# Performance work log

Measured on AMD Instinct MI355X. Metric: run time of the kernel, lower is better.

## Reference

```python
import jax, jax.numpy as jnp
from jax import lax
import numpy as np

IN, G, H, L = 128, 5, 512, 256   # input_size, n_genres, hidden_dim, latent_dim
E = 2 * H                         # encoder_hidden_dim (bidirectional)
B, T = 128, 256
SLOPE = 0.01                      # torch LeakyReLU default


def _gru(xt, h, Wih, Whh, bih, bhh):
    # torch.nn.GRUCell: gates ordered r, z, n
    gi = xt @ Wih.T + bih         # [B, 3H]
    gh = h @ Whh.T + bhh          # [B, 3H]
    ir, iz, inn = jnp.split(gi, 3, axis=-1)
    hr, hz, hn = jnp.split(gh, 3, axis=-1)
    r = jax.nn.sigmoid(ir + hr)
    z = jax.nn.sigmoid(iz + hz)
    n = jnp.tanh(inn + r * hn)
    return (1.0 - z) * n + z * h


def _leaky(v):
    return jnp.where(v >= 0, v, SLOPE * v)


def setup_inputs() -> dict:
    key = jax.random.key(0)
    ks = jax.random.split(key, 32)
    it = iter(range(32))

    def p(shape, fan_in):
        s = 1.0 / np.sqrt(fan_in)
        return jax.random.uniform(ks[next(it)], shape, jnp.float32, -s, s)

    inp = {
        "x": jax.random.normal(ks[next(it)], (B, T, IN + G), jnp.float32),
        "latent_genre_vec": jax.random.uniform(ks[next(it)], (B, G), jnp.float32),
        "eps": jax.random.normal(ks[next(it)], (B, L - G), jnp.float32),
    }
    # forward encoder GRUCell (input IN+G -> H)
    inp["Wih_e"] = p((3 * H, IN + G), H); inp["Whh_e"] = p((3 * H, H), H)
    inp["bih_e"] = p((3 * H,), H);        inp["bhh_e"] = p((3 * H,), H)
    # backward encoder GRUCell
    inp["Wih_be"] = p((3 * H, IN + G), H); inp["Whh_be"] = p((3 * H, H), H)
    inp["bih_be"] = p((3 * H,), H);        inp["bhh_be"] = p((3 * H,), H)
    # decoder GRUCell (input IN -> H)
    inp["Wih_d"] = p((3 * H, IN), H); inp["Whh_d"] = p((3 * H, H), H)
    inp["bih_d"] = p((3 * H,), H);    inp["bhh_d"] = p((3 * H,), H)
    # fc_mu: [Linear(E,E)+LeakyReLU, Linear(E, L-G)]
    inp["W_mu0"] = p((E, E), E); inp["b_mu0"] = p((E,), E)
    inp["W_mu1"] = p((L - G, E), E); inp["b_mu1"] = p((L - G,), E)
    # fc_logvar
    inp["W_lv0"] = p((E, E), E); inp["b_lv0"] = p((E,), E)
    inp["W_lv1"] = p((L - G, E), E); inp["b_lv1"] = p((L - G,), E)
    # fc_latent: [Linear(L,L)+LeakyReLU, Linear(L, H)]
    inp["W_lat0"] = p((L, L), L); inp["b_lat0"] = p((L,), L)
    inp["W_lat1"] = p((H, L), L); inp["b_lat1"] = p((H,), L)
    # fc_decoder final Linear(H, IN) (fc_decoder[0] is dead code in the original loop)
    inp["W_dec1"] = p((IN, H), H); inp["b_dec1"] = p((IN,), H)
    return inp


def reference(x, latent_genre_vec, eps,
              Wih_e, Whh_e, bih_e, bhh_e,
              Wih_be, Whh_be, bih_be, bhh_be,
              Wih_d, Whh_d, bih_d, bhh_d,
              W_mu0, b_mu0, W_mu1, b_mu1,
              W_lv0, b_lv0, W_lv1, b_lv1,
              W_lat0, b_lat0, W_lat1, b_lat1,
              W_dec1, b_dec1):
    b = x.shape[0]
    xs = jnp.swapaxes(x, 0, 1)  # [T, B, IN+G]
    h0 = jnp.zeros((b, H), x.dtype)

    def enc_step(h, xt):
        return _gru(xt, h, Wih_e, Whh_e, bih_e, bhh_e), None

    def benc_step(h, xt):
        return _gru(xt, h, Wih_be, Whh_be, bih_be, bhh_be), None

    h_fwd, _ = lax.scan(enc_step, h0, xs)
    h_bwd, _ = lax.scan(benc_step, h0, xs, reverse=True)
    hidden = jnp.concatenate([h_fwd, h_bwd], axis=1)  # [B, 2H]

    mu = _leaky(hidden @ W_mu0.T + b_mu0) @ W_mu1.T + b_mu1        # [B, L-G]
    logvar = _leaky(hidden @ W_lv0.T + b_lv0) @ W_lv1.T + b_lv1    # [B, L-G]

    z = mu + jnp.exp(0.5 * logvar) * eps
    z = jnp.concatenate([z, latent_genre_vec], axis=1)             # [B, L]

    dec_h = _leaky(z @ W_lat0.T + b_lat0) @ W_lat1.T + b_lat1      # [B, H]

    note0 = x[:, 0, :IN]  # [B, IN]

    def dec_step(carry, _):
        h, note = carry
        h = _gru(note, h, Wih_d, Whh_d, bih_d, bhh_d)
        # faithful to original: final fc_decoder layer applied to hidden
        note = h @ W_dec1.T + b_dec1
        return (h, note), note

    _, notes = lax.scan(dec_step, (dec_h, note0), None, length=x.shape[1] - 1)
    output = jnp.concatenate([note0[:, None, :], jnp.swapaxes(notes, 0, 1)], axis=1)  # [B, T, IN]
    return output, mu, logvar
```

## Files before the change

kernel.cpp:

```cpp
#include <hip/hip_runtime.h>

#define B_ 128
#define T_ 256
#define IN_ 128
#define G_ 5
#define H_ 512
#define G3_ 1536
#define E_ 1024
#define L_ 256
#define LG_ 251
#define INPG_ 133

#define MU_OFF (B_*T_*IN_)
#define LV_OFF (MU_OFF + B_*LG_)

typedef __attribute__((ext_vector_type(8))) short bf16x8;
typedef __attribute__((ext_vector_type(4))) float f32x4;
typedef unsigned long long u64;

__device__ __forceinline__ float bf2f(unsigned short s) {
    return __uint_as_float(((unsigned)s) << 16);
}
__device__ __forceinline__ unsigned short f2bf(float f) {
    unsigned x = __float_as_uint(f);
    unsigned r = (x + 0x7fffu + ((x >> 16) & 1u)) >> 16;
    return (unsigned short)r;
}
__device__ __forceinline__ float sigf(float v) {
    return 1.f / (1.f + __expf(-v));
}
__device__ __forceinline__ int ld_flag(const int* p) {
    return __hip_atomic_load(p, __ATOMIC_RELAXED, __HIP_MEMORY_SCOPE_AGENT);
}
__device__ __forceinline__ void st_flag(int* p, int v) {
    __hip_atomic_store(p, v, __ATOMIC_RELAXED, __HIP_MEMORY_SCOPE_AGENT);
}
__device__ __forceinline__ u64 ld_h64(const void* p) {
    return __hip_atomic_load((const u64*)p, __ATOMIC_RELAXED, __HIP_MEMORY_SCOPE_AGENT);
}
__device__ __forceinline__ void st_h32(void* p, unsigned v) {
    __hip_atomic_store((unsigned*)p, v, __ATOMIC_RELAXED, __HIP_MEMORY_SCOPE_AGENT);
}


__global__ void xpad_k(const float* __restrict__ x, ushort* __restrict__ xb) {
    int id = blockIdx.x * 256 + threadIdx.x;
    if (id >= T_ * B_ * 160) return;
    int t = id / (B_ * 160);
    int rem = id - t * (B_ * 160);
    int b = rem / 160, c = rem - b * 160;
    float v = (c < INPG_) ? x[((size_t)b * T_ + t) * INPG_ + c] : 0.f;
    xb[id] = f2bf(v);
}

__global__ void pack_we(const float* __restrict__ Wih_f, const float* __restrict__ Whh_f,
                        const float* __restrict__ Wih_b, const float* __restrict__ Whh_b,
                        ushort* __restrict__ WE) {
    int id = blockIdx.x * 256 + threadIdx.x;
    int lane = id & 63;
    int rest = id >> 6;
    int ks = rest % 63;
    int cb = (rest / 63) & 31;
    int dir = rest / (63 * 32);
    if (dir >= 2) return;
    const float* Wih = dir ? Wih_b : Wih_f;
    const float* Whh = dir ? Whh_b : Whh_f;
    int n = lane & 15, kb = lane >> 4;
    int p, ksp;
    if (ks < 21)      { p = 0; ksp = ks; }
    else if (ks < 42) { p = 1; ksp = ks - 21; }
    else if (ks < 47) { p = 2; ksp = ks - 42; }
    else              { p = 3; ksp = ks - 47; }
    int j = cb * 16 + n;
    int row = (p == 0) ? j : (p == 1) ? 512 + j : 1024 + j;
    #pragma unroll
    for (int e = 0; e < 8; ++e) {
        int k = ksp * 32 + kb * 8 + e;
        float v;
        if (p == 3)      v = Whh[(size_t)row * 512 + k];
        else if (p == 2) v = (k < INPG_) ? Wih[(size_t)row * INPG_ + k] : 0.f;
        else v = (k < INPG_) ? Wih[(size_t)row * INPG_ + k]
               : (k < 160)   ? 0.f
               : Whh[(size_t)row * 512 + (k - 160)];
        WE[(size_t)id * 8 + e] = f2bf(v);
    }
}

__global__ void wfused_k(const float* __restrict__ Wih_d, const float* __restrict__ Wdec1,
                         float* __restrict__ Wf) {
    int id = blockIdx.x * 256 + threadIdx.x;
    if (id >= G3_ * H_) return;
    int r = id >> 9, c = id & 511;
    float s = 0.f;
    for (int m = 0; m < 128; ++m)
        s += Wih_d[(size_t)r * 128 + m] * Wdec1[(size_t)m * 512 + c];
    Wf[id] = s;
}

__global__ void bfi_k(const float* __restrict__ Wih_d, const float* __restrict__ b_dec1,
                      const float* __restrict__ bih_d, float* __restrict__ bfi) {
    int r = blockIdx.x * 256 + threadIdx.x;
    if (r >= G3_) return;
    float s = bih_d[r];
    for (int m = 0; m < 128; ++m)
        s += Wih_d[(size_t)r * 128 + m] * b_dec1[m];
    bfi[r] = s;
}

__global__ void pack_wd(const float* __restrict__ Wf, const float* __restrict__ Whh,
                        ushort* __restrict__ WD, int fused) {
    int id = blockIdx.x * 256 + threadIdx.x;
    int lane = id & 63;
    int rest = id >> 6;
    int ks = rest & 63;
    int cb = rest >> 6;
    if (cb >= 32) return;
    int p = ks >> 4, ksp = ks & 15;
    int n = lane & 15, kb = lane >> 4;
    int j = cb * 16 + n;
    int row = (p == 0) ? j : (p == 1) ? 512 + j : 1024 + j;
    #pragma unroll
    for (int e = 0; e < 8; ++e) {
        int k = ksp * 32 + kb * 8 + e;
        float v;
        if (p <= 1) v = fused ? (Wf[(size_t)row * 512 + k] + Whh[(size_t)row * 512 + k])
                              : Whh[(size_t)row * 512 + k];
        else if (p == 2) v = fused ? Wf[(size_t)row * 512 + k] : 0.f;
        else v = Whh[(size_t)row * 512 + k];
        WD[(size_t)id * 8 + e] = f2bf(v);
    }
}

__global__ void pack_wdec(const float* __restrict__ Wdec1, ushort* __restrict__ pk) {
    int id = blockIdx.x * 256 + threadIdx.x;
    if (id >= 8192) return;
    int lane = id & 63, ch = id >> 6;
    int nt = ch >> 4, ks = ch & 15;
    int n = nt * 16 + (lane & 15);
    int k0 = ks * 32 + (lane >> 4) * 8;
    #pragma unroll
    for (int e = 0; e < 8; ++e)
        pk[(size_t)id * 8 + e] = f2bf(Wdec1[(size_t)n * 512 + k0 + e]);
}

__global__ void zero_init(ushort* __restrict__ hb, int* __restrict__ ef,
                          int* __restrict__ df) {
    int id = blockIdx.x * 256 + threadIdx.x;
    if (id < 4 * 65536) hb[id] = 0;
    if (id < 4096) ef[id] = 0;
    if (id < 2048) df[id] = 0;
}

__global__ void note0_k2(const float* __restrict__ x, float* __restrict__ out,
                         float* __restrict__ note0f) {
    int id = blockIdx.x * 256 + threadIdx.x;
    if (id >= B_ * IN_) return;
    int b = id >> 7, n = id & 127;
    float v = x[((size_t)b * T_) * INPG_ + n];
    out[((size_t)b * T_) * IN_ + n] = v;
    note0f[(size_t)b * 128 + n] = v;
}

__global__ void cvt_h0(const float* __restrict__ src, ushort* __restrict__ dst) {
    int id = blockIdx.x * 256 + threadIdx.x;
    if (id < B_ * H_) dst[id] = f2bf(src[id]);
}

__global__ void tile_w(const float* __restrict__ W, ushort4* __restrict__ out,
                       int N, int K, int KC) {
    int id = blockIdx.x * 256 + threadIdx.x;
    if (id >= KC * N) return;
    int kc = id / N, n = id - kc * N;
    int k = kc * 4;
    ushort4 u;
    u.x = f2bf(k + 0 < K ? W[(size_t)n * K + k + 0] : 0.f);
    u.y = f2bf(k + 1 < K ? W[(size_t)n * K + k + 1] : 0.f);
    u.z = f2bf(k + 2 < K ? W[(size_t)n * K + k + 2] : 0.f);
    u.w = f2bf(k + 3 < K ? W[(size_t)n * K + k + 3] : 0.f);
    out[(size_t)kc * N + n] = u;
}

__global__ __launch_bounds__(256) void enc_persist(
    const ushort* __restrict__ xb16, const ushort* __restrict__ WE,
    ushort* __restrict__ hb,
    float* __restrict__ hidden,
    const float* __restrict__ bih_f, const float* __restrict__ bhh_f,
    const float* __restrict__ bih_b, const float* __restrict__ bhh_b,
    int* __restrict__ flags)
{
    __shared__ ushort As[32 * 680];
    __shared__ ushort Ws[63 * 512];
    __shared__ float gs[4][512];
    int bid = blockIdx.x;
    int dir = bid >> 7, bt = (bid >> 5) & 3, cb = bid & 31;
    int b0 = bt * 32;
    int tid = threadIdx.x;
    const float* bih = dir ? bih_b : bih_f;
    const float* bhh = dir ? bhh_b : bhh_f;

    {
        const ushort* src = WE + (size_t)((dir * 32 + cb) * 63) * 512;
        for (int c = tid; c < 4032; c += 256)
            *(uint4*)&Ws[c * 8] = *(const uint4*)&src[c * 8];
    }
    int bA = tid >> 3;
    int j0 = cb * 16 + 2 * (tid & 7), j1 = j0 + 1;
    float b_r0 = bih[j0] + bhh[j0],        b_r1 = bih[j1] + bhh[j1];
    float b_z0 = bih[512 + j0] + bhh[512 + j0], b_z1 = bih[512 + j1] + bhh[512 + j1];
    float b_in0 = bih[1024 + j0],          b_in1 = bih[1024 + j1];
    float b_hn0 = bhh[1024 + j0],          b_hn1 = bhh[1024 + j1];
    float hc0 = 0.f, hc1 = 0.f;

    int lane = tid & 63, wv = tid >> 6;
    int m = lane & 15, kb = lane >> 4;
    int nk  = (wv == 2) ? 5 : (wv == 3) ? 16 : 21;
    int ksb = (wv == 0) ? 0 : (wv == 1) ? 21 : (wv == 2) ? 42 : 47;
    int kcol0 = (wv == 3) ? 160 : 0;
    int ai0 = m * 680 + kcol0 + kb * 8;
    int ai1 = (16 + m) * 680 + kcol0 + kb * 8;
    const int* fpoll = &flags[((bid & ~31) + (lane & 31)) * 16];

    auto stage_x = [&](int t2) {
        int tt2 = dir ? (255 - t2) : t2;
        const ushort* xr2 = xb16 + (size_t)tt2 * (B_ * 160);
        #pragma unroll
        for (int i = 0; i < 3; ++i) {
            int c = tid + i * 256;
            if (c < 640) {
                int row = c / 20, off = c - row * 20;
                *(uint4*)((char*)As + row * 1360 + off * 16) =
                    *(const uint4*)(xr2 + (size_t)(b0 + row) * 160 + off * 8);
            }
        }
    };
    stage_x(0);

    for (int t = 0; t < T_; ++t) {
        int pp = t & 1;
        const ushort* hin = hb + (size_t)(pp * 2 + dir) * 65536;
        ushort* hout = hb + (size_t)((pp ^ 1) * 2 + dir) * 65536;
        if (t > 0) {
            if (wv == 0)
                while (!__all(ld_flag(fpoll) >= t)) __builtin_amdgcn_s_sleep(1);
            __syncthreads();
        }
        {
            u64 vb[16];
            #pragma unroll
            for (int i = 0; i < 16; ++i) {
                int c = tid + i * 256;
                int row = c >> 7, off = c & 127;
                vb[i] = ld_h64(hin + (size_t)(b0 + row) * 512 + off * 4);
            }
            #pragma unroll
            for (int i = 0; i < 16; ++i) {
                int c = tid + i * 256;
                int row = c >> 7, off = c & 127;
                *(u64*)((char*)As + row * 1360 + 320 + off * 8) = vb[i];
            }
        }
        __syncthreads();
        f32x4 acc0 = {0.f,0.f,0.f,0.f}, acc1 = {0.f,0.f,0.f,0.f};
        const ushort* Bp = &Ws[ksb * 512 + lane * 8];
        for (int ks = 0; ks < nk; ++ks) {
            bf16x8 bfr = *(const bf16x8*)(Bp + (size_t)ks * 512);
            bf16x8 a0 = *(const bf16x8*)&As[ai0 + ks * 32];
            bf16x8 a1 = *(const bf16x8*)&As[ai1 + ks * 32];
            acc0 = __builtin_amdgcn_mfma_f32_16x16x32_bf16(a0, bfr, acc0, 0, 0, 0);
            acc1 = __builtin_amdgcn_mfma_f32_16x16x32_bf16(a1, bfr, acc1, 0, 0, 0);
        }
        #pragma unroll
        for (int i = 0; i < 4; ++i) {
            gs[wv][(kb * 4 + i) * 16 + m] = acc0[i];
            gs[wv][(16 + kb * 4 + i) * 16 + m] = acc1[i];
        }
        __syncthreads();
        {
            int o0 = 2 * tid, o1 = o0 + 1;
            float r0 = sigf(gs[0][o0] + b_r0);
            float z0 = sigf(gs[1][o0] + b_z0);
            float n0 = tanhf(gs[2][o0] + b_in0 + r0 * (gs[3][o0] + b_hn0));
            hc0 = (1.f - z0) * n0 + z0 * hc0;
            float r1 = sigf(gs[0][o1] + b_r1);
            float z1 = sigf(gs[1][o1] + b_z1);
            float n1 = tanhf(gs[2][o1] + b_in1 + r1 * (gs[3][o1] + b_hn1));
            hc1 = (1.f - z1) * n1 + z1 * hc1;
            unsigned pkd = (unsigned)f2bf(hc0) | ((unsigned)f2bf(hc1) << 16);
            st_h32((char*)hout + ((size_t)(b0 + bA) * 512 + j0) * 2, pkd);
            if (t == 255) {
                float2 hv = {hc0, hc1};
                *(float2*)&hidden[(size_t)(b0 + bA) * 1024 + dir * 512 + j0] = hv;
            }
        }
        __syncthreads();
        if (t < 255) {
            if (tid == 0) st_flag(&flags[bid * 16], t + 1);
            stage_x(t + 1);
        }
    }
}

__global__ __launch_bounds__(256) void dec_persist(
    const ushort* __restrict__ hdec0, const ushort* __restrict__ WD2,
    const ushort* __restrict__ WD1, ushort* __restrict__ hist,
    const float* __restrict__ h0f, const float* __restrict__ bfi,
    const float* __restrict__ bhh, const float* __restrict__ gi0,
    int* __restrict__ flags)
{
    __shared__ ushort As[32 * 520];
    __shared__ ushort Ws[64 * 512];
    __shared__ float gs[4][512];
    int bid = blockIdx.x;
    int bt = bid >> 5, cb = bid & 31;
    int b0 = bt * 32, tid = threadIdx.x;
    {
        const ushort* src = WD2 + (size_t)(cb * 64) * 512;
        for (int c = tid; c < 4096; c += 256)
            *(uint4*)&Ws[c * 8] = *(const uint4*)&src[c * 8];
    }
    int bA = tid >> 3;
    int j0 = cb * 16 + 2 * (tid & 7), j1 = j0 + 1;
    float f_r0 = bfi[j0] + bhh[j0],             f_r1 = bfi[j1] + bhh[j1];
    float f_z0 = bfi[512 + j0] + bhh[512 + j0], f_z1 = bfi[512 + j1] + bhh[512 + j1];
    float f_in0 = bfi[1024 + j0],               f_in1 = bfi[1024 + j1];
    float f_hn0 = bhh[1024 + j0],               f_hn1 = bhh[1024 + j1];
    float bh_r0 = bhh[j0], bh_r1 = bhh[j1];
    float bh_z0 = bhh[512 + j0], bh_z1 = bhh[512 + j1];
    float hc0 = h0f[(size_t)(b0 + bA) * 512 + j0];
    float hc1 = h0f[(size_t)(b0 + bA) * 512 + j1];
    float g0r = gi0[(size_t)(b0 + bA) * G3_ + j0];
    float g1r = gi0[(size_t)(b0 + bA) * G3_ + j1];
    float g0z = gi0[(size_t)(b0 + bA) * G3_ + 512 + j0];
    float g1z = gi0[(size_t)(b0 + bA) * G3_ + 512 + j1];
    float g0n = gi0[(size_t)(b0 + bA) * G3_ + 1024 + j0];
    float g1n = gi0[(size_t)(b0 + bA) * G3_ + 1024 + j1];

    int lane = tid & 63, wv = tid >> 6;
    int m = lane & 15, kb = lane >> 4;
    int ai0 = m * 520 + kb * 8, ai1 = (16 + m) * 520 + kb * 8;
    const ushort* WD1s = WD1 + (size_t)(cb * 64 + wv * 16) * 512 + lane * 8;
    const int* fpoll = &flags[((bid & ~31) + (lane & 31)) * 16];

    for (int t = 1; t < T_; ++t) {
        if (t >= 2) {
            if (wv == 0)
                while (!__all(ld_flag(fpoll) >= t - 1)) __builtin_amdgcn_s_sleep(1);
            __syncthreads();
        }
        const ushort* hsrc = (t == 1) ? hdec0 : hist + (size_t)(t - 2) * 65536;
        {
            u64 vb[16];
            #pragma unroll
            for (int i = 0; i < 16; ++i) {
                int c = tid + i * 256;
                int row = c >> 7, off = c & 127;
                vb[i] = ld_h64(hsrc + (size_t)(b0 + row) * 512 + off * 4);
            }
            #pragma unroll
            for (int i = 0; i < 16; ++i) {
                int c = tid + i * 256;
                int row = c >> 7, off = c & 127;
                *(u64*)((char*)As + row * 1040 + off * 8) = vb[i];
            }
        }
        __syncthreads();
        f32x4 acc0 = {0.f,0.f,0.f,0.f}, acc1 = {0.f,0.f,0.f,0.f};
        if (t == 1) {
            if (wv != 2) {
                for (int ks = 0; ks < 16; ++ks) {
                    bf16x8 bfr = *(const bf16x8*)(WD1s + (size_t)ks * 512);
                    bf16x8 a0 = *(const bf16x8*)&As[ai0 + ks * 32];
                    bf16x8 a1 = *(const bf16x8*)&As[ai1 + ks * 32];
                    acc0 = __builtin_amdgcn_mfma_f32_16x16x32_bf16(a0, bfr, acc0, 0, 0, 0);
                    acc1 = __builtin_amdgcn_mfma_f32_16x16x32_bf16(a1, bfr, acc1, 0, 0, 0);
                }
            }
        } else {
            const ushort* Bp = &Ws[(wv * 16) * 512 + lane * 8];
            for (int ks = 0; ks < 16; ++ks) {
                bf16x8 bfr = *(const bf16x8*)(Bp + (size_t)ks * 512);
                bf16x8 a0 = *(const bf16x8*)&As[ai0 + ks * 32];
                bf16x8 a1 = *(const bf16x8*)&As[ai1 + ks * 32];
                acc0 = __builtin_amdgcn_mfma_f32_16x16x32_bf16(a0, bfr, acc0, 0, 0, 0);
                acc1 = __builtin_amdgcn_mfma_f32_16x16x32_bf16(a1, bfr, acc1, 0, 0, 0);
            }
        }
        #pragma unroll
        for (int i = 0; i < 4; ++i) {
            gs[wv][(kb * 4 + i) * 16 + m] = acc0[i];
            gs[wv][(16 + kb * 4 + i) * 16 + m] = acc1[i];
        }
        __syncthreads();
        {
            int o0 = 2 * tid, o1 = o0 + 1;
            float r0, z0, n0, r1, z1, n1;
            if (t == 1) {
                r0 = sigf(gs[0][o0] + g0r + bh_r0);
                z0 = sigf(gs[1][o0] + g0z + bh_z0);
                n0 = tanhf(gs[2][o0] + g0n + r0 * (gs[3][o0] + f_hn0));
                r1 = sigf(gs[0][o1] + g1r + bh_r1);
                z1 = sigf(gs[1][o1] + g1z + bh_z1);
                n1 = tanhf(gs[2][o1] + g1n + r1 * (gs[3][o1] + f_hn1));
            } else {
                r0 = sigf(gs[0][o0] + f_r0);
                z0 = sigf(gs[1][o0] + f_z0);
                n0 = tanhf(gs[2][o0] + f_in0 + r0 * (gs[3][o0] + f_hn0));
                r1 = sigf(gs[0][o1] + f_r1);
                z1 = sigf(gs[1][o1] + f_z1);
                n1 = tanhf(gs[2][o1] + f_in1 + r1 * (gs[3][o1] + f_hn1));
            }
            hc0 = (1.f - z0) * n0 + z0 * hc0;
            hc1 = (1.f - z1) * n1 + z1 * hc1;
            unsigned pkd = (unsigned)f2bf(hc0) | ((unsigned)f2bf(hc1) << 16);
            st_h32((char*)(hist + (size_t)(t - 1) * 65536) +
                   ((size_t)(b0 + bA) * 512 + j0) * 2, pkd);
        }
        __syncthreads();
        if (t < 255 && tid == 0) st_flag(&flags[bid * 16], t);
    }
}

__global__ __launch_bounds__(256) void notes_mfma(
    const ushort* __restrict__ hist, const ushort* __restrict__ pk,
    const float* __restrict__ bd, float* __restrict__ out)
{
    __shared__ ushort hs[32 * 520];
    int m0 = blockIdx.x * 32;
    int tid = threadIdx.x;
    #pragma unroll
    for (int i = 0; i < 8; ++i) {
        int c = tid + i * 256;
        int row = c >> 6, off = c & 63;
        *(uint4*)((char*)hs + row * 1040 + off * 16) =
            *(const uint4*)(hist + (size_t)(m0 + row) * 512 + off * 8);
    }
    __syncthreads();
    int lane = tid & 63, wv = tid >> 6;
    int m = lane & 15, kb = lane >> 4;
    int nt0 = wv * 2;
    f32x4 acc00 = {0.f,0.f,0.f,0.f}, acc01 = {0.f,0.f,0.f,0.f};
    f32x4 acc10 = {0.f,0.f,0.f,0.f}, acc11 = {0.f,0.f,0.f,0.f};
    for (int ks = 0; ks < 16; ++ks) {
        bf16x8 a0 = *(const bf16x8*)&hs[m * 520 + ks * 32 + kb * 8];
        bf16x8 a1 = *(const bf16x8*)&hs[(16 + m) * 520 + ks * 32 + kb * 8];
        bf16x8 bf0 = *(const bf16x8*)&pk[(size_t)((nt0 * 16 + ks) * 64 + lane) * 8];
        bf16x8 bf1 = *(const bf16x8*)&pk[(size_t)(((nt0 + 1) * 16 + ks) * 64 + lane) * 8];
        acc00 = __builtin_amdgcn_mfma_f32_16x16x32_bf16(a0, bf0, acc00, 0, 0, 0);
        acc01 = __builtin_amdgcn_mfma_f32_16x16x32_bf16(a0, bf1, acc01, 0, 0, 0);
        acc10 = __builtin_amdgcn_mfma_f32_16x16x32_bf16(a1, bf0, acc10, 0, 0, 0);
        acc11 = __builtin_amdgcn_mfma_f32_16x16x32_bf16(a1, bf1, acc11, 0, 0, 0);
    }
    int n0 = nt0 * 16 + (lane & 15), n1 = (nt0 + 1) * 16 + (lane & 15);
    #pragma unroll
    for (int i = 0; i < 4; ++i) {
        int r0 = m0 + kb * 4 + i;
        int r1 = r0 + 16;
        int t0 = r0 >> 7, b0r = r0 & 127;
        int t1 = r1 >> 7, b1r = r1 & 127;
        out[((size_t)b0r * T_ + (t0 + 1)) * IN_ + n0] = acc00[i] + bd[n0];
        out[((size_t)b0r * T_ + (t0 + 1)) * IN_ + n1] = acc01[i] + bd[n1];
        out[((size_t)b1r * T_ + (t1 + 1)) * IN_ + n0] = acc10[i] + bd[n0];
        out[((size_t)b1r * T_ + (t1 + 1)) * IN_ + n1] = acc11[i] + bd[n1];
    }
}

__global__ __launch_bounds__(256) void gemm_t4(
    const float* __restrict__ A, const ushort4* __restrict__ Wt,
    const float* __restrict__ bias, float* __restrict__ C,
    int M, int N, int K, int act)
{
    int nb = blockIdx.x, mb = blockIdx.y;
    int tid = threadIdx.x;
    int n = nb * 64 + (tid & 63);
    int mq = tid >> 6;
    int m0 = mb * 32;
    __shared__ float Asm[32][36];
    float acc[8];
    #pragma unroll
    for (int i = 0; i < 8; ++i) acc[i] = 0.f;
    for (int k0 = 0; k0 < K; k0 += 32) {
        int r = tid >> 3, c = (tid & 7) << 2;
        float4 v = *(const float4*)&A[(size_t)(m0 + r) * K + k0 + c];
        Asm[r][c] = v.x; Asm[r][c+1] = v.y; Asm[r][c+2] = v.z; Asm[r][c+3] = v.w;
        __syncthreads();
        #pragma unroll
        for (int kc = 0; kc < 8; ++kc) {
            float w0 = 0.f, w1 = 0.f, w2 = 0.f, w3 = 0.f;
            if (n < N) {
                ushort4 u = Wt[(size_t)((k0 >> 2) + kc) * N + n];
                w0 = bf2f(u.x); w1 = bf2f(u.y); w2 = bf2f(u.z); w3 = bf2f(u.w);
            }
            #pragma unroll
            for (int i = 0; i < 8; ++i) {
                int mm = mq * 8 + i;
                acc[i] += Asm[mm][kc*4+0]*w0 + Asm[mm][kc*4+1]*w1
                        + Asm[mm][kc*4+2]*w2 + Asm[mm][kc*4+3]*w3;
            }
        }
        __syncthreads();
    }
    if (n < N) {
        #pragma unroll
        for (int i = 0; i < 8; ++i) {
            int mm = m0 + mq * 8 + i;
            float v = acc[i] + bias[n];
            if (act == 1) v = (v >= 0.f) ? v : 0.01f * v;
            C[(size_t)mm * N + n] = v;
        }
    }
}

__global__ void z_k(const float* __restrict__ out, const float* __restrict__ eps,
                    const float* __restrict__ genre, float* __restrict__ zc) {
    int id = blockIdx.x * 256 + threadIdx.x;
    if (id >= B_ * L_) return;
    int b = id >> 8, c = id & 255;
    float v;
    if (c < LG_) {
        float mu = out[MU_OFF + (size_t)b * LG_ + c];
        float lv = out[LV_OFF + (size_t)b * LG_ + c];
        v = mu + expf(0.5f * lv) * eps[(size_t)b * LG_ + c];
    } else {
        v = genre[(size_t)b * G_ + (c - LG_)];
    }
    zc[id] = v;
}

extern "C" void kernel_launch(void* const* d_in, const int* in_sizes, int n_in,
                              void* d_out, int out_size, void* d_ws, size_t ws_size,
                              hipStream_t stream) {
    (void)in_sizes; (void)n_in; (void)out_size; (void)ws_size;
    const float* x      = (const float*)d_in[0];
    const float* genre  = (const float*)d_in[1];
    const float* eps    = (const float*)d_in[2];
    const float* Wih_e  = (const float*)d_in[3];
    const float* Whh_e  = (const float*)d_in[4];
    const float* bih_e  = (const float*)d_in[5];
    const float* bhh_e  = (const float*)d_in[6];
    const float* Wih_be = (const float*)d_in[7];
    const float* Whh_be = (const float*)d_in[8];
    const float* bih_be = (const float*)d_in[9];
    const float* bhh_be = (const float*)d_in[10];
    const float* Wih_d  = (const float*)d_in[11];
    const float* Whh_d  = (const float*)d_in[12];
    const float* bih_d  = (const float*)d_in[13];
    const float* bhh_d  = (const float*)d_in[14];
    const float* W_mu0  = (const float*)d_in[15];
    const float* b_mu0  = (const float*)d_in[16];
    const float* W_mu1  = (const float*)d_in[17];
    const float* b_mu1  = (const float*)d_in[18];
    const float* W_lv0  = (const float*)d_in[19];
    const float* b_lv0  = (const float*)d_in[20];
    const float* W_lv1  = (const float*)d_in[21];
    const float* b_lv1  = (const float*)d_in[22];
    const float* W_lat0 = (const float*)d_in[23];
    const float* b_lat0 = (const float*)d_in[24];
    const float* W_lat1 = (const float*)d_in[25];
    const float* b_lat1 = (const float*)d_in[26];
    const float* W_dec1 = (const float*)d_in[27];
    const float* b_dec1 = (const float*)d_in[28];
    float* out = (float*)d_out;

    char* ws = (char*)d_ws;
    size_t off = 0;
    auto alloc = [&](size_t bytes) -> char* {
        char* p = ws + off;
        off = (off + bytes + 255) & ~(size_t)255;
        return p;
    };
    ushort* xb16  = (ushort*)alloc((size_t)T_ * B_ * 160 * 2);
    ushort* WE    = (ushort*)alloc((size_t)2 * 32 * 63 * 512 * 2);
    ushort* WD2   = (ushort*)alloc((size_t)32 * 64 * 512 * 2);
    ushort* WD1   = (ushort*)alloc((size_t)32 * 64 * 512 * 2);
    float*  Wf    = (float*)alloc((size_t)G3_ * H_ * 4);
    float*  bfi   = (float*)alloc(G3_ * 4);
    ushort* hb_e  = (ushort*)alloc((size_t)4 * 65536 * 2);
    ushort* hist  = (ushort*)alloc((size_t)255 * 65536 * 2);
    ushort* hdec0 = (ushort*)alloc((size_t)65536 * 2);
    ushort* pkdec = (ushort*)alloc((size_t)8192 * 8 * 2);
    int*    eflag = (int*)alloc((size_t)4096 * 4);
    int*    dflag = (int*)alloc((size_t)2048 * 4);
    float*  note0f= (float*)alloc((size_t)B_ * 128 * 4);
    float*  gi0   = (float*)alloc((size_t)B_ * G3_ * 4);
    float*  hidden= (float*)alloc((size_t)B_ * E_ * 4);
    float*  t0buf = (float*)alloc((size_t)B_ * E_ * 4);
    float*  t1buf = (float*)alloc((size_t)B_ * E_ * 4);
    float*  zcbuf = (float*)alloc((size_t)B_ * L_ * 4);
    float*  t2buf = (float*)alloc((size_t)B_ * L_ * 4);
    float*  t3buf = (float*)alloc((size_t)B_ * H_ * 4);

    ushort4* T_Wmu0  = (ushort4*)alloc((size_t)256 * E_ * 8);
    ushort4* T_Wmu1  = (ushort4*)alloc((size_t)256 * LG_ * 8);
    ushort4* T_Wlv0  = (ushort4*)alloc((size_t)256 * E_ * 8);
    ushort4* T_Wlv1  = (ushort4*)alloc((size_t)256 * LG_ * 8);
    ushort4* T_Wlat0 = (ushort4*)alloc((size_t)64 * L_ * 8);
    ushort4* T_Wlat1 = (ushort4*)alloc((size_t)64 * H_ * 8);
    ushort4* T_Wihd  = (ushort4*)alloc((size_t)32 * G3_ * 8);

    xpad_k<<<(T_ * B_ * 160 + 255) / 256, 256, 0, stream>>>(x, xb16);
    pack_we<<<1008, 256, 0, stream>>>(Wih_e, Whh_e, Wih_be, Whh_be, WE);
    wfused_k<<<(G3_ * H_ + 255) / 256, 256, 0, stream>>>(Wih_d, W_dec1, Wf);
    bfi_k<<<6, 256, 0, stream>>>(Wih_d, b_dec1, bih_d, bfi);
    pack_wd<<<512, 256, 0, stream>>>(Wf, Whh_d, WD2, 1);
    pack_wd<<<512, 256, 0, stream>>>(Wf, Whh_d, WD1, 0);
    pack_wdec<<<32, 256, 0, stream>>>(W_dec1, pkdec);
    zero_init<<<1024, 256, 0, stream>>>(hb_e, eflag, dflag);
    note0_k2<<<(B_ * IN_ + 255) / 256, 256, 0, stream>>>(x, out, note0f);

    auto tile = [&](const float* W, ushort4* dst, int N, int K) {
        int KC = (K + 3) / 4;
        tile_w<<<(KC * N + 255) / 256, 256, 0, stream>>>(W, dst, N, K, KC);
    };
    tile(W_mu0,  T_Wmu0,  E_,  E_);
    tile(W_mu1,  T_Wmu1,  LG_, E_);
    tile(W_lv0,  T_Wlv0,  E_,  E_);
    tile(W_lv1,  T_Wlv1,  LG_, E_);
    tile(W_lat0, T_Wlat0, L_,  L_);
    tile(W_lat1, T_Wlat1, H_,  L_);
    tile(Wih_d,  T_Wihd,  G3_, IN_);

    enc_persist<<<256, 256, 0, stream>>>(xb16, WE, hb_e, hidden,
                                         bih_e, bhh_e, bih_be, bhh_be, eflag);

    {
        dim3 g1(16, 4), g2(4, 4), g3(4, 4), g4(8, 4), g5(24, 4);
        gemm_t4<<<g1, 256, 0, stream>>>(hidden, T_Wmu0, b_mu0, t0buf, B_, E_, E_, 1);
        gemm_t4<<<g2, 256, 0, stream>>>(t0buf, T_Wmu1, b_mu1, out + MU_OFF, B_, LG_, E_, 0);
        gemm_t4<<<g1, 256, 0, stream>>>(hidden, T_Wlv0, b_lv0, t1buf, B_, E_, E_, 1);
        gemm_t4<<<g2, 256, 0, stream>>>(t1buf, T_Wlv1, b_lv1, out + LV_OFF, B_, LG_, E_, 0);
        z_k<<<(B_ * L_ + 255) / 256, 256, 0, stream>>>(out, eps, genre, zcbuf);
        gemm_t4<<<g3, 256, 0, stream>>>(zcbuf, T_Wlat0, b_lat0, t2buf, B_, L_, L_, 1);
        gemm_t4<<<g4, 256, 0, stream>>>(t2buf, T_Wlat1, b_lat1, t3buf, B_, H_, L_, 0);
        gemm_t4<<<g5, 256, 0, stream>>>(note0f, T_Wihd, bih_d, gi0, B_, G3_, IN_, 0);
    }
    cvt_h0<<<(B_ * H_ + 255) / 256, 256, 0, stream>>>(t3buf, hdec0);

    dec_persist<<<128, 256, 0, stream>>>(hdec0, WD2, WD1, hist, t3buf,
                                         bfi, bhh_d, gi0, dflag);

    notes_mfma<<<1020, 256, 0, stream>>>(hist, pkdec, b_dec1, out);
}
```

Baseline: 2.303 ms.

## Replace flag-based inter-block sync with poisoned-sentinel dataflow polling

Removes the per-step flag store and flag poll in the persistent encoder and decoder kernels. Each timestep now writes its hidden state into its own slot of a buffer that was pre-filled with all-ones bf16 (NaN) sentinels, and consumers spin on the data itself until no sentinel halfwords remain. The decoder's first step moves into a separate small kernel, and sigmoid/tanh switch to rcp-based fast approximations. The cost is a much larger poison-fill pass over a per-timestep history buffer, and the scheme hangs if a real value ever encodes as the sentinel pattern.

```diff
diff --git a/kernel.cpp b/kernel.cpp
--- a/kernel.cpp
+++ b/kernel.cpp
@@ -27,19 +27,22 @@
     return (unsigned short)r;
 }
 __device__ __forceinline__ float sigf(float v) {
-    return 1.f / (1.f + __expf(-v));
-}
-__device__ __forceinline__ int ld_flag(const int* p) {
-    return __hip_atomic_load(p, __ATOMIC_RELAXED, __HIP_MEMORY_SCOPE_AGENT);
-}
-__device__ __forceinline__ void st_flag(int* p, int v) {
-    __hip_atomic_store(p, v, __ATOMIC_RELAXED, __HIP_MEMORY_SCOPE_AGENT);
+    return __builtin_amdgcn_rcpf(1.f + __expf(-v));
+}
+__device__ __forceinline__ float ftanh(float x) {
+    x = fminf(15.f, fmaxf(-15.f, x));
+    float e = __expf(2.f * x);
+    return (e - 1.f) * __builtin_amdgcn_rcpf(e + 1.f);
 }
 __device__ __forceinline__ u64 ld_h64(const void* p) {
     return __hip_atomic_load((const u64*)p, __ATOMIC_RELAXED, __HIP_MEMORY_SCOPE_AGENT);
 }
 __device__ __forceinline__ void st_h32(void* p, unsigned v) {
     __hip_atomic_store((unsigned*)p, v, __ATOMIC_RELAXED, __HIP_MEMORY_SCOPE_AGENT);
+}
+__device__ __forceinline__ u64 badm(u64 v) {
+    u64 x = ~v;
+    return (x - 0x0001000100010001ull) & ~x & 0x8000800080008000ull;
 }
 
 
@@ -143,12 +146,11 @@
         pk[(size_t)id * 8 + e] = f2bf(Wdec1[(size_t)n * 512 + k0 + e]);
 }
 
-__global__ void zero_init(ushort* __restrict__ hb, int* __restrict__ ef,
-                          int* __restrict__ df) {
-    int id = blockIdx.x * 256 + threadIdx.x;
-    if (id < 4 * 65536) hb[id] = 0;
-    if (id < 4096) ef[id] = 0;
-    if (id < 2048) df[id] = 0;
+__global__ void poison_k(ulonglong2* __restrict__ hb, ulonglong2* __restrict__ hist) {
+    size_t id = (size_t)blockIdx.x * 256 + threadIdx.x;
+    ulonglong2 p; p.x = ~0ull; p.y = ~0ull;
+    if (id < (size_t)256 * 2 * 65536 / 8) hb[id] = p;
+    if (id < (size_t)255 * 65536 / 8)     hist[id] = p;
 }
 
 __global__ void note0_k2(const float* __restrict__ x, float* __restrict__ out,
@@ -180,13 +182,14 @@
     out[(size_t)kc * N + n] = u;
 }
 
+#define MFMA16(a, b, c) __builtin_amdgcn_mfma_f32_16x16x32_bf16((a), (b), (c), 0, 0, 0)
+
 __global__ __launch_bounds__(256) void enc_persist(
     const ushort* __restrict__ xb16, const ushort* __restrict__ WE,
     ushort* __restrict__ hb,
     float* __restrict__ hidden,
     const float* __restrict__ bih_f, const float* __restrict__ bhh_f,
-    const float* __restrict__ bih_b, const float* __restrict__ bhh_b,
-    int* __restrict__ flags)
+    const float* __restrict__ bih_b, const float* __restrict__ bhh_b)
 {
     __shared__ ushort As[32 * 680];
     __shared__ ushort Ws[63 * 512];
@@ -203,12 +206,28 @@
         for (int c = tid; c < 4032; c += 256)
             *(uint4*)&Ws[c * 8] = *(const uint4*)&src[c * 8];
     }
+    for (int i = 0; i < 16; ++i) {
+        int c = tid + i * 256;
+        int row = c >> 7, off = c & 127;
+        *(u64*)((char*)As + row * 1360 + 320 + off * 8) = 0ull;
+    }
+    {
+        const ushort* xr = xb16 + (size_t)(dir ? 255 : 0) * (B_ * 160);
+        for (int i = 0; i < 3; ++i) {
+            int c = tid + i * 256;
+            if (c < 640) {
+                int row = c / 20, off = c - row * 20;
+                *(uint4*)((char*)As + row * 1360 + off * 16) =
+                    *(const uint4*)(xr + (size_t)(b0 + row) * 160 + off * 8);
+            }
+        }
+    }
     int bA = tid >> 3;
     int j0 = cb * 16 + 2 * (tid & 7), j1 = j0 + 1;
-    float b_r0 = bih[j0] + bhh[j0],        b_r1 = bih[j1] + bhh[j1];
+    float b_r0 = bih[j0] + bhh[j0],             b_r1 = bih[j1] + bhh[j1];
     float b_z0 = bih[512 + j0] + bhh[512 + j0], b_z1 = bih[512 + j1] + bhh[512 + j1];
-    float b_in0 = bih[1024 + j0],          b_in1 = bih[1024 + j1];
-    float b_hn0 = bhh[1024 + j0],          b_hn1 = bhh[1024 + j1];
+    float b_in0 = bih[1024 + j0],               b_in1 = bih[1024 + j1];
+    float b_hn0 = bhh[1024 + j0],               b_hn1 = bhh[1024 + j1];
     float hc0 = 0.f, hc1 = 0.f;
 
     int lane = tid & 63, wv = tid >> 6;
@@ -218,39 +237,24 @@
     int kcol0 = (wv == 3) ? 160 : 0;
     int ai0 = m * 680 + kcol0 + kb * 8;
     int ai1 = (16 + m) * 680 + kcol0 + kb * 8;
-    const int* fpoll = &flags[((bid & ~31) + (lane & 31)) * 16];
-
-    auto stage_x = [&](int t2) {
-        int tt2 = dir ? (255 - t2) : t2;
-        const ushort* xr2 = xb16 + (size_t)tt2 * (B_ * 160);
-        #pragma unroll
-        for (int i = 0; i < 3; ++i) {
-            int c = tid + i * 256;
-            if (c < 640) {
-                int row = c / 20, off = c - row * 20;
-                *(uint4*)((char*)As + row * 1360 + off * 16) =
-                    *(const uint4*)(xr2 + (size_t)(b0 + row) * 160 + off * 8);
-            }
-        }
-    };
-    stage_x(0);
+    int hrow = tid >> 3, hoff = (tid & 7);
 
     for (int t = 0; t < T_; ++t) {
-        int pp = t & 1;
-        const ushort* hin = hb + (size_t)(pp * 2 + dir) * 65536;
-        ushort* hout = hb + (size_t)((pp ^ 1) * 2 + dir) * 65536;
+        ushort* hout = hb + ((size_t)t * 2 + dir) * 65536;
         if (t > 0) {
-            if (wv == 0)
-                while (!__all(ld_flag(fpoll) >= t)) __builtin_amdgcn_s_sleep(1);
-            __syncthreads();
-        }
-        {
+            const ushort* hin = hb + ((size_t)(t - 1) * 2 + dir) * 65536;
             u64 vb[16];
-            #pragma unroll
-            for (int i = 0; i < 16; ++i) {
-                int c = tid + i * 256;
-                int row = c >> 7, off = c & 127;
-                vb[i] = ld_h64(hin + (size_t)(b0 + row) * 512 + off * 4);
+            for (;;) {
+                #pragma unroll
+                for (int i = 0; i < 16; ++i) {
+                    int c = tid + i * 256;
+                    int row = c >> 7, off = c & 127;
+                    vb[i] = ld_h64(hin + (size_t)(b0 + row) * 512 + off * 4);
+                }
+                u64 bad = 0;
+                #pragma unroll
+                for (int i = 0; i < 16; ++i) bad |= badm(vb[i]);
+                if (__all(bad == 0)) break;
             }
             #pragma unroll
             for (int i = 0; i < 16; ++i) {
@@ -266,8 +270,8 @@
             bf16x8 bfr = *(const bf16x8*)(Bp + (size_t)ks * 512);
             bf16x8 a0 = *(const bf16x8*)&As[ai0 + ks * 32];
             bf16x8 a1 = *(const bf16x8*)&As[ai1 + ks * 32];
-            acc0 = __builtin_amdgcn_mfma_f32_16x16x32_bf16(a0, bfr, acc0, 0, 0, 0);
-            acc1 = __builtin_amdgcn_mfma_f32_16x16x32_bf16(a1, bfr, acc1, 0, 0, 0);
+            acc0 = MFMA16(a0, bfr, acc0);
+            acc1 = MFMA16(a1, bfr, acc1);
         }
         #pragma unroll
         for (int i = 0; i < 4; ++i) {
@@ -279,33 +283,81 @@
             int o0 = 2 * tid, o1 = o0 + 1;
             float r0 = sigf(gs[0][o0] + b_r0);
             float z0 = sigf(gs[1][o0] + b_z0);
-            float n0 = tanhf(gs[2][o0] + b_in0 + r0 * (gs[3][o0] + b_hn0));
+            float n0 = ftanh(gs[2][o0] + b_in0 + r0 * (gs[3][o0] + b_hn0));
             hc0 = (1.f - z0) * n0 + z0 * hc0;
             float r1 = sigf(gs[0][o1] + b_r1);
             float z1 = sigf(gs[1][o1] + b_z1);
-            float n1 = tanhf(gs[2][o1] + b_in1 + r1 * (gs[3][o1] + b_hn1));
+            float n1 = ftanh(gs[2][o1] + b_in1 + r1 * (gs[3][o1] + b_hn1));
             hc1 = (1.f - z1) * n1 + z1 * hc1;
             unsigned pkd = (unsigned)f2bf(hc0) | ((unsigned)f2bf(hc1) << 16);
             st_h32((char*)hout + ((size_t)(b0 + bA) * 512 + j0) * 2, pkd);
-            if (t == 255) {
-                float2 hv = {hc0, hc1};
-                *(float2*)&hidden[(size_t)(b0 + bA) * 1024 + dir * 512 + j0] = hv;
+        }
+        if (t == 255) {
+            float2 hv = {hc0, hc1};
+            *(float2*)&hidden[(size_t)(b0 + bA) * 1024 + dir * 512 + j0] = hv;
+        } else {
+            int tt2 = dir ? (254 - t) : (t + 1);
+            const ushort* xr2 = xb16 + (size_t)tt2 * (B_ * 160);
+            for (int i2 = 0; i2 < 3; ++i2) {
+                int c = tid + i2 * 256;
+                if (c < 640) {
+                    int row = c / 20, off2 = c - row * 20;
+                    *(uint4*)((char*)As + row * 1360 + off2 * 16) =
+                        *(const uint4*)(xr2 + (size_t)(b0 + row) * 160 + off2 * 8);
+                }
             }
         }
-        __syncthreads();
-        if (t < 255) {
-            if (tid == 0) st_flag(&flags[bid * 16], t + 1);
-            stage_x(t + 1);
-        }
+    }
+    (void)hrow; (void)hoff;
+}
+
+__global__ __launch_bounds__(64, 1) void dec_step1(
+    const ushort* __restrict__ hdec0, const ushort* __restrict__ WD1,
+    const float* __restrict__ h0f, const float* __restrict__ gi0,
+    const float* __restrict__ bhh, ushort* __restrict__ hist0,
+    float* __restrict__ h1f)
+{
+    int bid = blockIdx.x;
+    int rt = bid >> 5, cb = bid & 31;
+    int lane = threadIdx.x;
+    int m = lane & 15, kb = lane >> 4;
+    int arow = rt * 16 + m;
+    int j = cb * 16 + m;
+    int orow = rt * 16 + kb * 4;
+    const ushort* hr = hdec0 + (size_t)arow * 512 + kb * 8;
+    bf16x8 af[16];
+    #pragma unroll
+    for (int ks = 0; ks < 16; ++ks)
+        af[ks] = *(const bf16x8*)(hr + ks * 32);
+    const ushort* w1 = WD1 + (size_t)(cb * 64) * 512 + lane * 8;
+    f32x4 aR = {0.f,0.f,0.f,0.f}, aZ = {0.f,0.f,0.f,0.f}, aGh = {0.f,0.f,0.f,0.f};
+    #pragma unroll
+    for (int ks = 0; ks < 16; ++ks) {
+        aR = MFMA16(af[ks], *(const bf16x8*)(w1 + (size_t)ks * 512), aR);
+        aZ = MFMA16(af[ks], *(const bf16x8*)(w1 + (size_t)(16 + ks) * 512), aZ);
+        aGh = MFMA16(af[ks], *(const bf16x8*)(w1 + (size_t)(48 + ks) * 512), aGh);
+    }
+    float bh_r = bhh[j], bh_z = bhh[512 + j], bh_n = bhh[1024 + j];
+    #pragma unroll
+    for (int i = 0; i < 4; ++i) {
+        int rg = orow + i;
+        float gr = gi0[(size_t)rg * G3_ + j];
+        float gz = gi0[(size_t)rg * G3_ + 512 + j];
+        float gn = gi0[(size_t)rg * G3_ + 1024 + j];
+        float h0 = h0f[(size_t)rg * 512 + j];
+        float r = sigf(aR[i] + gr + bh_r);
+        float z = sigf(aZ[i] + gz + bh_z);
+        float n = ftanh(gn + r * (aGh[i] + bh_n));
+        float h1 = (1.f - z) * n + z * h0;
+        h1f[(size_t)rg * 512 + j] = h1;
+        hist0[(size_t)rg * 512 + j] = f2bf(h1);
     }
 }
 
 __global__ __launch_bounds__(256) void dec_persist(
-    const ushort* __restrict__ hdec0, const ushort* __restrict__ WD2,
-    const ushort* __restrict__ WD1, ushort* __restrict__ hist,
-    const float* __restrict__ h0f, const float* __restrict__ bfi,
-    const float* __restrict__ bhh, const float* __restrict__ gi0,
-    int* __restrict__ flags)
+    const ushort* __restrict__ WD2, ushort* __restrict__ hist,
+    const float* __restrict__ h1f, const float* __restrict__ bfi,
+    const float* __restrict__ bhh)
 {
     __shared__ ushort As[32 * 520];
     __shared__ ushort Ws[64 * 512];
@@ -324,66 +376,43 @@
     float f_z0 = bfi[512 + j0] + bhh[512 + j0], f_z1 = bfi[512 + j1] + bhh[512 + j1];
     float f_in0 = bfi[1024 + j0],               f_in1 = bfi[1024 + j1];
     float f_hn0 = bhh[1024 + j0],               f_hn1 = bhh[1024 + j1];
-    float bh_r0 = bhh[j0], bh_r1 = bhh[j1];
-    float bh_z0 = bhh[512 + j0], bh_z1 = bhh[512 + j1];
-    float hc0 = h0f[(size_t)(b0 + bA) * 512 + j0];
-    float hc1 = h0f[(size_t)(b0 + bA) * 512 + j1];
-    float g0r = gi0[(size_t)(b0 + bA) * G3_ + j0];
-    float g1r = gi0[(size_t)(b0 + bA) * G3_ + j1];
-    float g0z = gi0[(size_t)(b0 + bA) * G3_ + 512 + j0];
-    float g1z = gi0[(size_t)(b0 + bA) * G3_ + 512 + j1];
-    float g0n = gi0[(size_t)(b0 + bA) * G3_ + 1024 + j0];
-    float g1n = gi0[(size_t)(b0 + bA) * G3_ + 1024 + j1];
+    float hc0 = h1f[(size_t)(b0 + bA) * 512 + j0];
+    float hc1 = h1f[(size_t)(b0 + bA) * 512 + j1];
 
     int lane = tid & 63, wv = tid >> 6;
     int m = lane & 15, kb = lane >> 4;
     int ai0 = m * 520 + kb * 8, ai1 = (16 + m) * 520 + kb * 8;
-    const ushort* WD1s = WD1 + (size_t)(cb * 64 + wv * 16) * 512 + lane * 8;
-    const int* fpoll = &flags[((bid & ~31) + (lane & 31)) * 16];
-
-    for (int t = 1; t < T_; ++t) {
-        if (t >= 2) {
-            if (wv == 0)
-                while (!__all(ld_flag(fpoll) >= t - 1)) __builtin_amdgcn_s_sleep(1);
-            __syncthreads();
-        }
-        const ushort* hsrc = (t == 1) ? hdec0 : hist + (size_t)(t - 2) * 65536;
-        {
-            u64 vb[16];
+
+    for (int t = 2; t < T_; ++t) {
+        const ushort* hin = hist + (size_t)(t - 2) * 65536;
+        u64 vb[16];
+        for (;;) {
             #pragma unroll
             for (int i = 0; i < 16; ++i) {
                 int c = tid + i * 256;
                 int row = c >> 7, off = c & 127;
-                vb[i] = ld_h64(hsrc + (size_t)(b0 + row) * 512 + off * 4);
+                vb[i] = ld_h64(hin + (size_t)(b0 + row) * 512 + off * 4);
             }
+            u64 bad = 0;
             #pragma unroll
-            for (int i = 0; i < 16; ++i) {
-                int c = tid + i * 256;
-                int row = c >> 7, off = c & 127;
-                *(u64*)((char*)As + row * 1040 + off * 8) = vb[i];
-            }
+            for (int i = 0; i < 16; ++i) bad |= badm(vb[i]);
+            if (__all(bad == 0)) break;
+        }
+        #pragma unroll
+        for (int i = 0; i < 16; ++i) {
+            int c = tid + i * 256;
+            int row = c >> 7, off = c & 127;
+            *(u64*)((char*)As + row * 1040 + off * 8) = vb[i];
         }
         __syncthreads();
         f32x4 acc0 = {0.f,0.f,0.f,0.f}, acc1 = {0.f,0.f,0.f,0.f};
-        if (t == 1) {
-            if (wv != 2) {
-                for (int ks = 0; ks < 16; ++ks) {
-                    bf16x8 bfr = *(const bf16x8*)(WD1s + (size_t)ks * 512);
-                    bf16x8 a0 = *(const bf16x8*)&As[ai0 + ks * 32];
-                    bf16x8 a1 = *(const bf16x8*)&As[ai1 + ks * 32];
-                    acc0 = __builtin_amdgcn_mfma_f32_16x16x32_bf16(a0, bfr, acc0, 0, 0, 0);
-                    acc1 = __builtin_amdgcn_mfma_f32_16x16x32_bf16(a1, bfr, acc1, 0, 0, 0);
-                }
-            }
-        } else {
-            const ushort* Bp = &Ws[(wv * 16) * 512 + lane * 8];
-            for (int ks = 0; ks < 16; ++ks) {
-                bf16x8 bfr = *(const bf16x8*)(Bp + (size_t)ks * 512);
-                bf16x8 a0 = *(const bf16x8*)&As[ai0 + ks * 32];
-                bf16x8 a1 = *(const bf16x8*)&As[ai1 + ks * 32];
-                acc0 = __builtin_amdgcn_mfma_f32_16x16x32_bf16(a0, bfr, acc0, 0, 0, 0);
-                acc1 = __builtin_amdgcn_mfma_f32_16x16x32_bf16(a1, bfr, acc1, 0, 0, 0);
-            }
+        const ushort* Bp = &Ws[(wv * 16) * 512 + lane * 8];
+        for (int ks = 0; ks < 16; ++ks) {
+            bf16x8 bfr = *(const bf16x8*)(Bp + (size_t)ks * 512);
+            bf16x8 a0 = *(const bf16x8*)&As[ai0 + ks * 32];
+            bf16x8 a1 = *(const bf16x8*)&As[ai1 + ks * 32];
+            acc0 = MFMA16(a0, bfr, acc0);
+            acc1 = MFMA16(a1, bfr, acc1);
         }
         #pragma unroll
         for (int i = 0; i < 4; ++i) {
@@ -393,30 +422,18 @@
         __syncthreads();
         {
             int o0 = 2 * tid, o1 = o0 + 1;
-            float r0, z0, n0, r1, z1, n1;
-            if (t == 1) {
-                r0 = sigf(gs[0][o0] + g0r + bh_r0);
-                z0 = sigf(gs[1][o0] + g0z + bh_z0);
-                n0 = tanhf(gs[2][o0] + g0n + r0 * (gs[3][o0] + f_hn0));
-                r1 = sigf(gs[0][o1] + g1r + bh_r1);
-                z1 = sigf(gs[1][o1] + g1z + bh_z1);
-                n1 = tanhf(gs[2][o1] + g1n + r1 * (gs[3][o1] + f_hn1));
-            } else {
-                r0 = sigf(gs[0][o0] + f_r0);
-                z0 = sigf(gs[1][o0] + f_z0);
-                n0 = tanhf(gs[2][o0] + f_in0 + r0 * (gs[3][o0] + f_hn0));
-                r1 = sigf(gs[0][o1] + f_r1);
-                z1 = sigf(gs[1][o1] + f_z1);
-                n1 = tanhf(gs[2][o1] + f_in1 + r1 * (gs[3][o1] + f_hn1));
-            }
+            float r0 = sigf(gs[0][o0] + f_r0);
+            float z0 = sigf(gs[1][o0] + f_z0);
+            float n0 = ftanh(gs[2][o0] + f_in0 + r0 * (gs[3][o0] + f_hn0));
             hc0 = (1.f - z0) * n0 + z0 * hc0;
+            float r1 = sigf(gs[0][o1] + f_r1);
+            float z1 = sigf(gs[1][o1] + f_z1);
+            float n1 = ftanh(gs[2][o1] + f_in1 + r1 * (gs[3][o1] + f_hn1));
             hc1 = (1.f - z1) * n1 + z1 * hc1;
             unsigned pkd = (unsigned)f2bf(hc0) | ((unsigned)f2bf(hc1) << 16);
             st_h32((char*)(hist + (size_t)(t - 1) * 65536) +
                    ((size_t)(b0 + bA) * 512 + j0) * 2, pkd);
         }
-        __syncthreads();
-        if (t < 255 && tid == 0) st_flag(&flags[bid * 16], t);
     }
 }
 
@@ -445,10 +462,10 @@
         bf16x8 a1 = *(const bf16x8*)&hs[(16 + m) * 520 + ks * 32 + kb * 8];
         bf16x8 bf0 = *(const bf16x8*)&pk[(size_t)((nt0 * 16 + ks) * 64 + lane) * 8];
         bf16x8 bf1 = *(const bf16x8*)&pk[(size_t)(((nt0 + 1) * 16 + ks) * 64 + lane) * 8];
-        acc00 = __builtin_amdgcn_mfma_f32_16x16x32_bf16(a0, bf0, acc00, 0, 0, 0);
-        acc01 = __builtin_amdgcn_mfma_f32_16x16x32_bf16(a0, bf1, acc01, 0, 0, 0);
-        acc10 = __builtin_amdgcn_mfma_f32_16x16x32_bf16(a1, bf0, acc10, 0, 0, 0);
-        acc11 = __builtin_amdgcn_mfma_f32_16x16x32_bf16(a1, bf1, acc11, 0, 0, 0);
+        acc00 = MFMA16(a0, bf0, acc00);
+        acc01 = MFMA16(a0, bf1, acc01);
+        acc10 = MFMA16(a1, bf0, acc10);
+        acc11 = MFMA16(a1, bf1, acc11);
     }
     int n0 = nt0 * 16 + (lane & 15), n1 = (nt0 + 1) * 16 + (lane & 15);
     #pragma unroll
@@ -574,12 +591,10 @@
     ushort* WD1   = (ushort*)alloc((size_t)32 * 64 * 512 * 2);
     float*  Wf    = (float*)alloc((size_t)G3_ * H_ * 4);
     float*  bfi   = (float*)alloc(G3_ * 4);
-    ushort* hb_e  = (ushort*)alloc((size_t)4 * 65536 * 2);
+    ushort* hb_e  = (ushort*)alloc((size_t)256 * 2 * 65536 * 2);
     ushort* hist  = (ushort*)alloc((size_t)255 * 65536 * 2);
     ushort* hdec0 = (ushort*)alloc((size_t)65536 * 2);
     ushort* pkdec = (ushort*)alloc((size_t)8192 * 8 * 2);
-    int*    eflag = (int*)alloc((size_t)4096 * 4);
-    int*    dflag = (int*)alloc((size_t)2048 * 4);
     float*  note0f= (float*)alloc((size_t)B_ * 128 * 4);
     float*  gi0   = (float*)alloc((size_t)B_ * G3_ * 4);
     float*  hidden= (float*)alloc((size_t)B_ * E_ * 4);
@@ -588,6 +603,7 @@
     float*  zcbuf = (float*)alloc((size_t)B_ * L_ * 4);
     float*  t2buf = (float*)alloc((size_t)B_ * L_ * 4);
     float*  t3buf = (float*)alloc((size_t)B_ * H_ * 4);
+    float*  h1f   = (float*)alloc((size_t)B_ * H_ * 4);
 
     ushort4* T_Wmu0  = (ushort4*)alloc((size_t)256 * E_ * 8);
     ushort4* T_Wmu1  = (ushort4*)alloc((size_t)256 * LG_ * 8);
@@ -604,7 +620,7 @@
     pack_wd<<<512, 256, 0, stream>>>(Wf, Whh_d, WD2, 1);
     pack_wd<<<512, 256, 0, stream>>>(Wf, Whh_d, WD1, 0);
     pack_wdec<<<32, 256, 0, stream>>>(W_dec1, pkdec);
-    zero_init<<<1024, 256, 0, stream>>>(hb_e, eflag, dflag);
+    poison_k<<<16384, 256, 0, stream>>>((ulonglong2*)hb_e, (ulonglong2*)hist);
     note0_k2<<<(B_ * IN_ + 255) / 256, 256, 0, stream>>>(x, out, note0f);
 
     auto tile = [&](const float* W, ushort4* dst, int N, int K) {
@@ -620,7 +636,7 @@
     tile(Wih_d,  T_Wihd,  G3_, IN_);
 
     enc_persist<<<256, 256, 0, stream>>>(xb16, WE, hb_e, hidden,
-                                         bih_e, bhh_e, bih_be, bhh_be, eflag);
+                                         bih_e, bhh_e, bih_be, bhh_be);
 
     {
         dim3 g1(16, 4), g2(4, 4), g3(4, 4), g4(8, 4), g5(24, 4);
@@ -635,8 +651,8 @@
     }
     cvt_h0<<<(B_ * H_ + 255) / 256, 256, 0, stream>>>(t3buf, hdec0);
 
-    dec_persist<<<128, 256, 0, stream>>>(hdec0, WD2, WD1, hist, t3buf,
-                                         bfi, bhh_d, gi0, dflag);
+    dec_step1<<<256, 64, 0, stream>>>(hdec0, WD1, t3buf, gi0, bhh_d, hist, h1f);
+    dec_persist<<<128, 256, 0, stream>>>(WD2, hist, h1f, bfi, bhh_d);
 
     notes_mfma<<<1020, 256, 0, stream>>>(hist, pkdec, b_dec1, out);
 }
```

After: 2.221 ms. -3.6%, faster.
